# Optimization experiments

Hardware: AMD Instinct MI355X
Metric: run time of the kernel (lower is better)

Reference implementation:

```python
import jax, jax.numpy as jnp
import numpy as np

B, S, D = 8, 2048, 64
NEG = -1e9


def setup_inputs() -> dict:
    key = jax.random.key(0)
    kq, kk, kv = jax.random.split(key, 3)
    return {
        "queries": jax.random.normal(kq, (B, S, D), dtype=jnp.float32),
        "keys": jax.random.normal(kk, (B, S, D), dtype=jnp.float32),
        "values": jax.random.normal(kv, (B, S, D), dtype=jnp.float32),
        "mask_q": jnp.ones((B, S), dtype=jnp.float32),
        "mask_k": jnp.ones((B, S), dtype=jnp.float32),
        "mask_v": jnp.ones((B, S), dtype=jnp.float32),
    }


def reference(queries, keys, values, mask_q, mask_k, mask_v):
    # scaled QK^T: [B, Sq, Sk]
    scaler = jnp.sqrt(jnp.asarray(queries.shape[-1], dtype=queries.dtype))
    scores = jnp.einsum("bqd,bkd->bqk", queries, keys) / scaler
    # additive padding mask from outer product of query/key masks
    padding_mask = mask_q[:, :, None] * mask_k[:, None, :]  # [B, Sq, Sk]
    scores = scores + (1.0 - padding_mask) * NEG
    attention_weights = jax.nn.softmax(scores, axis=-1)
    # mask values then weighted sum
    values = values * mask_v[:, :, None]
    output = jnp.einsum("bqk,bkd->bqd", attention_weights, values)
    return output
```

## Files before the change

### kernel.cpp

```cpp
#include <hip/hip_runtime.h>
#include <hip/hip_bf16.h>
#include <math.h>

#define BATCH 8
#define SEQ   2048
#define DIM   64
#define NEGC  (-1e9f)
#define SPLIT 4
#define TPB   8

typedef short short8  __attribute__((ext_vector_type(8)));
typedef float f32x4   __attribute__((ext_vector_type(4)));
typedef float f32x16  __attribute__((ext_vector_type(16)));

#define MFMA32(a, b, c) __builtin_amdgcn_mfma_f32_32x32x16_bf16((a), (b), (c), 0, 0, 0)

__device__ __forceinline__ ushort f2bf(float x) {
    uint u = __float_as_uint(x);
    uint r = (u + 0x7fffu + ((u >> 16) & 1u)) >> 16;
    return (ushort)r;
}
__device__ __forceinline__ float bf2f(ushort h) {
    return __uint_as_float(((uint)h) << 16);
}

__global__ __launch_bounds__(256)
void prep_kv(const float* __restrict__ K, const float* __restrict__ V,
             const float* __restrict__ MV, ushort* __restrict__ ws) {
    __shared__ float raw[64 * 68];
    const int t    = threadIdx.x;
    const int b    = blockIdx.x >> 5;
    const int tile = blockIdx.x & 31;
    const float* Kb  = K  + ((size_t)b * SEQ + tile * 64) * DIM;
    const float* Vb  = V  + ((size_t)b * SEQ + tile * 64) * DIM;
    const float* MVb = MV + (size_t)b * SEQ + tile * 64;
    ushort* wsI = ws + (size_t)(b * 32 + tile) * 8192;

#pragma unroll
    for (int u = 0; u < 4; u++) {
        int f = t + 256 * u, key = f >> 4, d4 = (f & 15) * 4;
        *(float4*)&raw[key * 68 + d4] = *(const float4*)(Kb + (size_t)f * 4);
    }
    __syncthreads();
#pragma unroll
    for (int u = 0; u < 2; u++) {
        int r = t + 256 * u;
        int mt = r >> 8, kc = (r >> 6) & 3, L = r & 63;
        int key = mt * 32 + (L & 31), d0 = kc * 16 + (L >> 5) * 8;
        float4 x0 = *(float4*)&raw[key * 68 + d0];
        float4 x1 = *(float4*)&raw[key * 68 + d0 + 4];
        float xs[8] = {x0.x, x0.y, x0.z, x0.w, x1.x, x1.y, x1.z, x1.w};
        short8 hv;
#pragma unroll
        for (int j = 0; j < 8; j++) hv[j] = (short)f2bf(xs[j]);
        *(short8*)(wsI + r * 8) = hv;
    }
    __syncthreads();

#pragma unroll
    for (int u = 0; u < 4; u++) {
        int f = t + 256 * u, key = f >> 4, d4 = (f & 15) * 4;
        float4 x = *(const float4*)(Vb + (size_t)f * 4);
        float mv = MVb[key];
        x.x *= mv; x.y *= mv; x.z *= mv; x.w *= mv;
        *(float4*)&raw[key * 68 + d4] = x;
    }
    __syncthreads();
#pragma unroll
    for (int u = 0; u < 2; u++) {
        int r = t + 256 * u;
        int dt = r >> 8, kc = (r >> 6) & 3, L = r & 63;
        int d = dt * 32 + (L & 31), k0 = kc * 16 + (L >> 5) * 8;
        short8 ov;
#pragma unroll
        for (int j = 0; j < 8; j++) ov[j] = (short)f2bf(raw[(k0 + j) * 68 + d]);
        *(short8*)(wsI + 4096 + r * 8) = ov;
    }
}

__global__ __launch_bounds__(256, 4)
void attn_main(const float* __restrict__ Q, const float* __restrict__ MQ,
               const float* __restrict__ MK, const ushort* __restrict__ ws,
               float* __restrict__ PO, float* __restrict__ ML) {
    __shared__ __align__(16) ushort Stage[2][8192];

    const int t    = threadIdx.x;
    const int w    = t >> 6;
    const int lane = t & 63;
    const int h    = lane >> 5;
    const int lm   = lane & 31;
    const int qg   = w & 1;
    const int kh   = w >> 1;

    const int s  = blockIdx.x & 3;
    const int qb = blockIdx.x >> 2;
    const int b  = qb >> 5;
    const int qt = qb & 31;
    const int q  = qt * 64 + qg * 32 + lm;

    const float*  MKb  = MK + (size_t)b * SEQ;
    const ushort* wsKV = ws + (size_t)b * 32 * 8192;

    short8 qh[4], ql[4];
    {
        const float* Qr = Q + ((size_t)b * SEQ + q) * DIM;
#pragma unroll
        for (int kc = 0; kc < 4; kc++) {
            const float* p = Qr + kc * 16 + h * 8;
            float4 x0 = *(const float4*)p;
            float4 x1 = *(const float4*)(p + 4);
            float xs[8] = {x0.x, x0.y, x0.z, x0.w, x1.x, x1.y, x1.z, x1.w};
#pragma unroll
            for (int j = 0; j < 8; j++) {
                float v   = xs[j] * 0.125f;
                ushort hi = f2bf(v);
                ql[kc][j] = (short)f2bf(v - bf2f(hi));
                qh[kc][j] = (short)hi;
            }
        }
    }
    const float mq   = MQ[(size_t)b * SEQ + q];
    const float apen = NEGC * mq;

    float m = -1e30f, l = 0.0f;
    f32x16 ot0, ot1;
#pragma unroll
    for (int i = 0; i < 16; i++) { ot0[i] = 0.0f; ot1[i] = 0.0f; }

    {
        const ushort* src = wsKV + (size_t)(s * TPB) * 8192;
#pragma unroll
        for (int u = 0; u < 4; u++) {
            const int off = (u * 256 + w * 64 + lane) * 8;
            __builtin_amdgcn_global_load_lds(
                (const __attribute__((address_space(1))) void*)(src + off),
                (__attribute__((address_space(3))) void*)(&Stage[0][0] + off),
                16, 0, 0);
        }
    }
    __syncthreads();

    f32x4 mk[4];
#pragma unroll
    for (int v = 0; v < 4; v++)
        mk[v] = *(const f32x4*)(MKb + (s * TPB) * 64 + kh * 32 + v * 8 + h * 4);

#pragma unroll 1
    for (int tt = 0; tt < TPB; tt++) {
        const ushort* cur = &Stage[tt & 1][0];

        if (tt + 1 < TPB) {
            const ushort* src = wsKV + (size_t)(s * TPB + tt + 1) * 8192;
            ushort* dst = &Stage[(tt + 1) & 1][0];
#pragma unroll
            for (int u = 0; u < 4; u++) {
                const int off = (u * 256 + w * 64 + lane) * 8;
                __builtin_amdgcn_global_load_lds(
                    (const __attribute__((address_space(1))) void*)(src + off),
                    (__attribute__((address_space(3))) void*)(dst + off),
                    16, 0, 0);
            }
        }
        f32x4 nmk[4];
#pragma unroll
        for (int v = 0; v < 4; v++) nmk[v] = mk[v];
        if (tt + 1 < TPB) {
            const float* mkp = MKb + (s * TPB + tt + 1) * 64 + kh * 32 + h * 4;
#pragma unroll
            for (int v = 0; v < 4; v++) nmk[v] = *(const f32x4*)(mkp + v * 8);
        }

        f32x16 st;
#pragma unroll
        for (int i = 0; i < 16; i++) st[i] = 0.0f;
#pragma unroll
        for (int kc = 0; kc < 4; kc++) {
            short8 a = *(const short8*)&cur[((kh * 4 + kc) * 64 + lane) * 8];
            st = MFMA32(a, qh[kc], st);
            st = MFMA32(a, ql[kc], st);
        }

        float sv[16];
#pragma unroll
        for (int v = 0; v < 4; v++)
#pragma unroll
            for (int c = 0; c < 4; c++)
                sv[v * 4 + c] = st[v * 4 + c] + (NEGC - apen * mk[v][c]);
        float cm = sv[0];
#pragma unroll
        for (int i = 1; i < 16; i++) cm = fmaxf(cm, sv[i]);
        cm = fmaxf(cm, __shfl_xor(cm, 32));
        float nm    = fmaxf(m, cm);
        float alpha = __expf(m - nm);
        m = nm;

        float p[16], cs = 0.0f;
#pragma unroll
        for (int i = 0; i < 16; i++) { p[i] = __expf(sv[i] - nm); cs += p[i]; }
        cs += __shfl_xor(cs, 32);
        l   = l * alpha + cs;
        ot0 *= alpha; ot1 *= alpha;

        uint g[4][2], x[4][2];
#pragma unroll
        for (int v = 0; v < 4; v++) {
            __hip_bfloat162 c0 = __float22bfloat162_rn(make_float2(p[v*4+0], p[v*4+1]));
            __hip_bfloat162 c1 = __float22bfloat162_rn(make_float2(p[v*4+2], p[v*4+3]));
            __builtin_memcpy(&g[v][0], &c0, 4);
            __builtin_memcpy(&g[v][1], &c1, 4);
            x[v][0] = (uint)__shfl_xor((int)g[v][0], 32);
            x[v][1] = (uint)__shfl_xor((int)g[v][1], 32);
        }
        uint pbw[2][4];
        pbw[0][0] = h ? x[1][0] : g[0][0];
        pbw[0][1] = h ? x[1][1] : g[0][1];
        pbw[0][2] = h ? g[1][0] : x[0][0];
        pbw[0][3] = h ? g[1][1] : x[0][1];
        pbw[1][0] = h ? x[3][0] : g[2][0];
        pbw[1][1] = h ? x[3][1] : g[2][1];
        pbw[1][2] = h ? g[3][0] : x[2][0];
        pbw[1][3] = h ? g[3][1] : x[2][1];

#pragma unroll
        for (int c = 0; c < 2; c++) {
            short8 pb;
            __builtin_memcpy(&pb, &pbw[c][0], 16);
            short8 v0 = *(const short8*)&cur[4096 + ((0 * 4 + kh * 2 + c) * 64 + lane) * 8];
            short8 v1 = *(const short8*)&cur[4096 + ((1 * 4 + kh * 2 + c) * 64 + lane) * 8];
            ot0 = MFMA32(v0, pb, ot0);
            ot1 = MFMA32(v1, pb, ot1);
        }

#pragma unroll
        for (int v = 0; v < 4; v++) mk[v] = nmk[v];
        __syncthreads();
    }

    float* MscF = (float*)&Stage[0][0];
    if (kh == 1) {
        float* sc = MscF + (qg * 64 + lane) * 36;
#pragma unroll
        for (int i = 0; i < 16; i++) { sc[i] = ot0[i]; sc[16 + i] = ot1[i]; }
        sc[32] = m;
        sc[33] = l;
    }
    __syncthreads();
    if (kh == 0) {
        const float* sc = MscF + (qg * 64 + lane) * 36;
        float mb = sc[32], lb = sc[33];
        float nm = fmaxf(m, mb);
        float fa = __expf(m - nm);
        float fb = __expf(mb - nm);
        float lt = l * fa + lb * fb;

        float* po = PO + (((size_t)(s * 8 + b) * SEQ) + qt * 64 + qg * 32 + lm) * 64;
#pragma unroll
        for (int dt = 0; dt < 2; dt++) {
            const f32x16& o = dt ? ot1 : ot0;
#pragma unroll
            for (int rq = 0; rq < 4; rq++) {
                f32x4 r;
#pragma unroll
                for (int c = 0; c < 4; c++)
                    r[c] = o[rq * 4 + c] * fa + sc[dt * 16 + rq * 4 + c] * fb;
                *(f32x4*)(po + dt * 32 + rq * 8 + h * 4) = r;
            }
        }
        if (h == 0) {
            float2* ml2 = (float2*)ML;
            ml2[((size_t)(s * 8 + b) * SEQ) + qt * 64 + qg * 32 + lm] =
                make_float2(nm, lt);
        }
    }
}

__global__ __launch_bounds__(256)
void merge_o(const float* __restrict__ PO, const float* __restrict__ ML,
             float* __restrict__ O) {
    const int tid = blockIdx.x * 256 + threadIdx.x;
    const int qln = tid >> 4;
    const int dq  = tid & 15;
    const int b   = qln >> 11;
    const int qr  = qln & 2047;

    const float2* ml2 = (const float2*)ML;
    const size_t MLS = (size_t)8 * SEQ;
    float2 mls[SPLIT];
#pragma unroll
    for (int s = 0; s < SPLIT; s++) mls[s] = ml2[(size_t)(s * 8 + b) * SEQ + qr];
    float mm = mls[0].x;
#pragma unroll
    for (int s = 1; s < SPLIT; s++) mm = fmaxf(mm, mls[s].x);
    float f[SPLIT], denom = 0.0f;
#pragma unroll
    for (int s = 0; s < SPLIT; s++) {
        f[s] = __expf(mls[s].x - mm);
        denom += mls[s].y * f[s];
    }
    float inv = 1.0f / denom;

    const size_t POS = (size_t)8 * SEQ * 64;
    const size_t o0  = ((size_t)b * SEQ + qr) * 64 + dq * 4;
    f32x4 acc = {0, 0, 0, 0};
#pragma unroll
    for (int s = 0; s < SPLIT; s++)
        acc += (*(const f32x4*)(PO + s * POS + o0)) * f[s];
    *(f32x4*)(O + ((size_t)b * SEQ + qr) * DIM + dq * 4) = acc * inv;
    (void)MLS;
}

extern "C" void kernel_launch(void* const* d_in, const int* in_sizes, int n_in,
                              void* d_out, int out_size, void* d_ws, size_t ws_size,
                              hipStream_t stream) {
    const float* Q  = (const float*)d_in[0];
    const float* K  = (const float*)d_in[1];
    const float* V  = (const float*)d_in[2];
    const float* MQ = (const float*)d_in[3];
    const float* MK = (const float*)d_in[4];
    const float* MV = (const float*)d_in[5];
    float* O = (float*)d_out;

    ushort* wsKV = (ushort*)d_ws;
    float*  PO   = (float*)((char*)d_ws + (4u << 20));
    float*  ML   = (float*)((char*)d_ws + (20u << 20));

    prep_kv  <<<dim3(256),  dim3(256), 0, stream>>>(K, V, MV, wsKV);
    attn_main<<<dim3(1024), dim3(256), 0, stream>>>(Q, MQ, MK, wsKV, PO, ML);
    merge_o  <<<dim3(1024), dim3(256), 0, stream>>>(PO, ML, O);
}
```

Before: 101.8 us.

## Split K/V prep into separate blocks, reorder attention grid, use nontemporal stores

```diff
diff --git a/kernel.cpp b/kernel.cpp
--- a/kernel.cpp
+++ b/kernel.cpp
@@ -29,52 +29,55 @@
              const float* __restrict__ MV, ushort* __restrict__ ws) {
     __shared__ float raw[64 * 68];
     const int t    = threadIdx.x;
-    const int b    = blockIdx.x >> 5;
-    const int tile = blockIdx.x & 31;
-    const float* Kb  = K  + ((size_t)b * SEQ + tile * 64) * DIM;
-    const float* Vb  = V  + ((size_t)b * SEQ + tile * 64) * DIM;
-    const float* MVb = MV + (size_t)b * SEQ + tile * 64;
+    const int isV  = blockIdx.x >> 8;
+    const int img  = blockIdx.x & 255;
+    const int b    = img >> 5;
+    const int tile = img & 31;
     ushort* wsI = ws + (size_t)(b * 32 + tile) * 8192;
 
-#pragma unroll
-    for (int u = 0; u < 4; u++) {
-        int f = t + 256 * u, key = f >> 4, d4 = (f & 15) * 4;
-        *(float4*)&raw[key * 68 + d4] = *(const float4*)(Kb + (size_t)f * 4);
-    }
-    __syncthreads();
-#pragma unroll
-    for (int u = 0; u < 2; u++) {
-        int r = t + 256 * u;
-        int mt = r >> 8, kc = (r >> 6) & 3, L = r & 63;
-        int key = mt * 32 + (L & 31), d0 = kc * 16 + (L >> 5) * 8;
-        float4 x0 = *(float4*)&raw[key * 68 + d0];
-        float4 x1 = *(float4*)&raw[key * 68 + d0 + 4];
-        float xs[8] = {x0.x, x0.y, x0.z, x0.w, x1.x, x1.y, x1.z, x1.w};
-        short8 hv;
-#pragma unroll
-        for (int j = 0; j < 8; j++) hv[j] = (short)f2bf(xs[j]);
-        *(short8*)(wsI + r * 8) = hv;
-    }
-    __syncthreads();
-
-#pragma unroll
-    for (int u = 0; u < 4; u++) {
-        int f = t + 256 * u, key = f >> 4, d4 = (f & 15) * 4;
-        float4 x = *(const float4*)(Vb + (size_t)f * 4);
-        float mv = MVb[key];
-        x.x *= mv; x.y *= mv; x.z *= mv; x.w *= mv;
-        *(float4*)&raw[key * 68 + d4] = x;
-    }
-    __syncthreads();
-#pragma unroll
-    for (int u = 0; u < 2; u++) {
-        int r = t + 256 * u;
-        int dt = r >> 8, kc = (r >> 6) & 3, L = r & 63;
-        int d = dt * 32 + (L & 31), k0 = kc * 16 + (L >> 5) * 8;
-        short8 ov;
-#pragma unroll
-        for (int j = 0; j < 8; j++) ov[j] = (short)f2bf(raw[(k0 + j) * 68 + d]);
-        *(short8*)(wsI + 4096 + r * 8) = ov;
+    if (!isV) {
+        const float* Kb = K + ((size_t)b * SEQ + tile * 64) * DIM;
+#pragma unroll
+        for (int u = 0; u < 4; u++) {
+            int f = t + 256 * u, key = f >> 4, d4 = (f & 15) * 4;
+            *(float4*)&raw[key * 68 + d4] = *(const float4*)(Kb + (size_t)f * 4);
+        }
+        __syncthreads();
+#pragma unroll
+        for (int u = 0; u < 2; u++) {
+            int r = t + 256 * u;
+            int mt = r >> 8, kc = (r >> 6) & 3, L = r & 63;
+            int key = mt * 32 + (L & 31), d0 = kc * 16 + (L >> 5) * 8;
+            float4 x0 = *(float4*)&raw[key * 68 + d0];
+            float4 x1 = *(float4*)&raw[key * 68 + d0 + 4];
+            float xs[8] = {x0.x, x0.y, x0.z, x0.w, x1.x, x1.y, x1.z, x1.w};
+            short8 hv;
+#pragma unroll
+            for (int j = 0; j < 8; j++) hv[j] = (short)f2bf(xs[j]);
+            *(short8*)(wsI + r * 8) = hv;
+        }
+    } else {
+        const float* Vb  = V  + ((size_t)b * SEQ + tile * 64) * DIM;
+        const float* MVb = MV + (size_t)b * SEQ + tile * 64;
+#pragma unroll
+        for (int u = 0; u < 4; u++) {
+            int f = t + 256 * u, key = f >> 4, d4 = (f & 15) * 4;
+            float4 x = *(const float4*)(Vb + (size_t)f * 4);
+            float mv = MVb[key];
+            x.x *= mv; x.y *= mv; x.z *= mv; x.w *= mv;
+            *(float4*)&raw[key * 68 + d4] = x;
+        }
+        __syncthreads();
+#pragma unroll
+        for (int u = 0; u < 2; u++) {
+            int r = t + 256 * u;
+            int dt = r >> 8, kc = (r >> 6) & 3, L = r & 63;
+            int d = dt * 32 + (L & 31), k0 = kc * 16 + (L >> 5) * 8;
+            short8 ov;
+#pragma unroll
+            for (int j = 0; j < 8; j++) ov[j] = (short)f2bf(raw[(k0 + j) * 68 + d]);
+            *(short8*)(wsI + 4096 + r * 8) = ov;
+        }
     }
 }
 
@@ -92,10 +95,10 @@
     const int qg   = w & 1;
     const int kh   = w >> 1;
 
-    const int s  = blockIdx.x & 3;
-    const int qb = blockIdx.x >> 2;
-    const int b  = qb >> 5;
-    const int qt = qb & 31;
+    const int b  = blockIdx.x & 7;
+    const int r  = blockIdx.x >> 3;
+    const int s  = r & 3;
+    const int qt = r >> 2;
     const int q  = qt * 64 + qg * 32 + lm;
 
     const float*  MKb  = MK + (size_t)b * SEQ;
@@ -259,17 +262,17 @@
             const f32x16& o = dt ? ot1 : ot0;
 #pragma unroll
             for (int rq = 0; rq < 4; rq++) {
-                f32x4 r;
+                f32x4 rv;
 #pragma unroll
                 for (int c = 0; c < 4; c++)
-                    r[c] = o[rq * 4 + c] * fa + sc[dt * 16 + rq * 4 + c] * fb;
-                *(f32x4*)(po + dt * 32 + rq * 8 + h * 4) = r;
+                    rv[c] = o[rq * 4 + c] * fa + sc[dt * 16 + rq * 4 + c] * fb;
+                __builtin_nontemporal_store(rv, (f32x4*)(po + dt * 32 + rq * 8 + h * 4));
             }
         }
         if (h == 0) {
-            float2* ml2 = (float2*)ML;
-            ml2[((size_t)(s * 8 + b) * SEQ) + qt * 64 + qg * 32 + lm] =
-                make_float2(nm, lt);
+            float* mlp = ML + 2 * (((size_t)(s * 8 + b) * SEQ) + qt * 64 + qg * 32 + lm);
+            __builtin_nontemporal_store(nm, mlp + 0);
+            __builtin_nontemporal_store(lt, mlp + 1);
         }
     }
 }
@@ -283,11 +286,12 @@
     const int b   = qln >> 11;
     const int qr  = qln & 2047;
 
-    const float2* ml2 = (const float2*)ML;
-    const size_t MLS = (size_t)8 * SEQ;
     float2 mls[SPLIT];
 #pragma unroll
-    for (int s = 0; s < SPLIT; s++) mls[s] = ml2[(size_t)(s * 8 + b) * SEQ + qr];
+    for (int s = 0; s < SPLIT; s++) {
+        const float* mlp = ML + 2 * ((size_t)(s * 8 + b) * SEQ + qr);
+        mls[s] = make_float2(mlp[0], mlp[1]);
+    }
     float mm = mls[0].x;
 #pragma unroll
     for (int s = 1; s < SPLIT; s++) mm = fmaxf(mm, mls[s].x);
@@ -303,10 +307,11 @@
     const size_t o0  = ((size_t)b * SEQ + qr) * 64 + dq * 4;
     f32x4 acc = {0, 0, 0, 0};
 #pragma unroll
-    for (int s = 0; s < SPLIT; s++)
-        acc += (*(const f32x4*)(PO + s * POS + o0)) * f[s];
+    for (int s = 0; s < SPLIT; s++) {
+        f32x4 v = __builtin_nontemporal_load((const f32x4*)(PO + s * POS + o0));
+        acc += v * f[s];
+    }
     *(f32x4*)(O + ((size_t)b * SEQ + qr) * DIM + dq * 4) = acc * inv;
-    (void)MLS;
 }
 
 extern "C" void kernel_launch(void* const* d_in, const int* in_sizes, int n_in,
@@ -324,7 +329,7 @@
     float*  PO   = (float*)((char*)d_ws + (4u << 20));
     float*  ML   = (float*)((char*)d_ws + (20u << 20));
 
-    prep_kv  <<<dim3(256),  dim3(256), 0, stream>>>(K, V, MV, wsKV);
+    prep_kv  <<<dim3(512),  dim3(256), 0, stream>>>(K, V, MV, wsKV);
     attn_main<<<dim3(1024), dim3(256), 0, stream>>>(Q, MQ, MK, wsKV, PO, ML);
     merge_o  <<<dim3(1024), dim3(256), 0, stream>>>(PO, ML, O);
 }
```

After: 105.4 us. 1.04x slower.
